# Kernel tuning notes

Measured on AMD Instinct MI355X. Metric: run time of the kernel, lower is better.

The kernel has to match this reference:

```python
import jax, jax.numpy as jnp
import numpy as np

N = 100000  # nodes
E = 1600000  # edges

def gcn_layer(x, W, b, src, tgt, ew):
    # support = x @ W + b ; messages gathered at src, weighted scatter-sum into tgt
    h = x @ W + b                      # [N, F_out]
    msg = h[src] * ew[:, None]         # [E, F_out]
    return jax.ops.segment_sum(msg, tgt, num_segments=N)  # [N, F_out]

def setup_inputs() -> dict:
    key = jax.random.key(0)
    ks = jax.random.split(key, 12)
    nfeat, nhid, nclass = 256, 128, 40
    x = jax.random.normal(ks[0], (N, nfeat), dtype=jnp.float32)
    src = jax.random.randint(ks[1], (E,), 0, N)
    tgt = jax.random.randint(ks[2], (E,), 0, N)
    edge_weight = jax.random.uniform(ks[3], (E,), dtype=jnp.float32)
    def w(k, fi, fo):
        return jax.random.normal(k, (fi, fo), dtype=jnp.float32) / np.sqrt(fi)
    return {
        "x": x, "src": src, "tgt": tgt, "edge_weight": edge_weight,
        "W0": w(ks[4], nfeat, nhid), "b0": jnp.zeros((nhid,), jnp.float32),
        "W1": w(ks[5], nhid, nhid),  "b1": jnp.zeros((nhid,), jnp.float32),
        "W2": w(ks[6], nhid, nhid),  "b2": jnp.zeros((nhid,), jnp.float32),
        "W3": w(ks[7], nhid, nclass),"b3": jnp.zeros((nclass,), jnp.float32),
    }

def reference(x, src, tgt, edge_weight, W0, b0, W1, b1, W2, b2, W3, b3):
    # RESK2 with nlayers=4, eval mode (dropout = identity).
    # x0 = relu(gc0); r = x0; x1 = relu(gc1); x2 = relu(gc2) + r; out = log_softmax(gc3)
    x0 = jax.nn.relu(gcn_layer(x, W0, b0, src, tgt, edge_weight))
    r = x0
    x1 = jax.nn.relu(gcn_layer(x0, W1, b1, src, tgt, edge_weight))
    x2 = jax.nn.relu(gcn_layer(x1, W2, b2, src, tgt, edge_weight)) + r
    logits = gcn_layer(x2, W3, b3, src, tgt, edge_weight)
    return jax.nn.log_softmax(logits, axis=1)
```

## Files before the change

### kernel.cpp

```cpp
#include <hip/hip_runtime.h>
#include <hip/hip_bf16.h>


typedef __attribute__((ext_vector_type(8))) short short8;
typedef __attribute__((ext_vector_type(4))) float float4v;

#define SC_SHIFT 8
#define SC_NODES 256
#define FILL_CAP 12288
#define SRC_MASK 0x1FFFF

static __device__ __forceinline__ float bf2f_lo(unsigned int v) {
    return __uint_as_float(v << 16);
}
static __device__ __forceinline__ float bf2f_hi(unsigned int v) {
    return __uint_as_float(v & 0xffff0000u);
}
static __device__ __forceinline__ unsigned short f2bf(float f) {
    unsigned int u = __float_as_uint(f);
    u = (u + 0x7fffu + ((u >> 16) & 1u)) >> 16;
    return (unsigned short)u;
}
static __device__ __forceinline__ unsigned int packbf(float a, float b) {
    return (unsigned int)f2bf(a) | ((unsigned int)f2bf(b) << 16);
}
static __device__ __forceinline__ float pw_w(unsigned int pe) {
    return __uint_as_float((pe >> 17) << 16);
}

static __device__ __forceinline__ void acc8(float* acc, uint4 v, float wt) {
    acc[0] = fmaf(bf2f_lo(v.x), wt, acc[0]);
    acc[1] = fmaf(bf2f_hi(v.x), wt, acc[1]);
    acc[2] = fmaf(bf2f_lo(v.y), wt, acc[2]);
    acc[3] = fmaf(bf2f_hi(v.y), wt, acc[3]);
    acc[4] = fmaf(bf2f_lo(v.z), wt, acc[4]);
    acc[5] = fmaf(bf2f_hi(v.z), wt, acc[5]);
    acc[6] = fmaf(bf2f_lo(v.w), wt, acc[6]);
    acc[7] = fmaf(bf2f_hi(v.w), wt, acc[7]);
}
static __device__ __forceinline__ void acc4(float* acc, uint2 v, float wt) {
    acc[0] = fmaf(bf2f_lo(v.x), wt, acc[0]);
    acc[1] = fmaf(bf2f_hi(v.x), wt, acc[1]);
    acc[2] = fmaf(bf2f_lo(v.y), wt, acc[2]);
    acc[3] = fmaf(bf2f_hi(v.y), wt, acc[3]);
}

__global__ __launch_bounds__(256) void k_count(const int* __restrict__ tgt,
                                               int* __restrict__ chunkTot,
                                               int E, int NSC) {
    __shared__ int hist[512];
    const int tid = threadIdx.x;
    hist[tid] = 0;
    hist[tid + 256] = 0;
    __syncthreads();
#pragma unroll
    for (int r = 0; r < 4; r++) {
        int e = blockIdx.x * 4096 + r * 1024 + tid * 4;
        if (e + 3 < E) {
            int4 tv = *(const int4*)&tgt[e];
            atomicAdd(&hist[tv.x >> SC_SHIFT], 1);
            atomicAdd(&hist[tv.y >> SC_SHIFT], 1);
            atomicAdd(&hist[tv.z >> SC_SHIFT], 1);
            atomicAdd(&hist[tv.w >> SC_SHIFT], 1);
        } else {
            for (int j = 0; j < 4; j++)
                if (e + j < E) atomicAdd(&hist[tgt[e + j] >> SC_SHIFT], 1);
        }
    }
    __syncthreads();
    for (int i = tid; i < NSC; i += 256) {
        int c = hist[i];
        if (c) atomicAdd(&chunkTot[i], c);
    }
}

__global__ __launch_bounds__(512) void k_scanB(const int* __restrict__ chunkTot,
                                               int* __restrict__ chunkStart,
                                               int* __restrict__ chunkCur,
                                               int E, int NSC) {
    __shared__ int sm[512];
    const int tid = threadIdx.x;
    int v = (tid < NSC) ? chunkTot[tid] : 0;
    sm[tid] = v;
    __syncthreads();
    for (int off = 1; off < 512; off <<= 1) {
        int t = (tid >= off) ? sm[tid - off] : 0;
        __syncthreads();
        sm[tid] += t;
        __syncthreads();
    }
    int excl = sm[tid] - v;
    if (tid < NSC) {
        chunkStart[tid] = excl;
        chunkCur[tid * 32] = excl;
    }
    if (tid == 0) chunkStart[NSC] = E;
}

__global__ __launch_bounds__(512) void k_bucket(const int* __restrict__ src,
                                                const int* __restrict__ tgt,
                                                const float* __restrict__ ew,
                                                int* __restrict__ chunkCur,
                                                unsigned int* __restrict__ st_pw,
                                                unsigned char* __restrict__ st_t8,
                                                int E) {
    __shared__ int cnt[512];
    __shared__ int rk[512];
    __shared__ int bbase[512];
    const int tid = threadIdx.x;
    cnt[tid] = 0;
    rk[tid] = 0;
    __syncthreads();

    int t16[16];
    unsigned int p16[16];
#pragma unroll
    for (int r = 0; r < 4; r++) {
        int e = blockIdx.x * 8192 + r * 2048 + tid * 4;
        if (e + 3 < E) {
            int4 tv = *(const int4*)&tgt[e];
            int4 sv = *(const int4*)&src[e];
            float4 wv = *(const float4*)&ew[e];
            t16[r * 4 + 0] = tv.x; t16[r * 4 + 1] = tv.y;
            t16[r * 4 + 2] = tv.z; t16[r * 4 + 3] = tv.w;
            p16[r * 4 + 0] = ((unsigned int)f2bf(wv.x) << 17) | (unsigned int)sv.x;
            p16[r * 4 + 1] = ((unsigned int)f2bf(wv.y) << 17) | (unsigned int)sv.y;
            p16[r * 4 + 2] = ((unsigned int)f2bf(wv.z) << 17) | (unsigned int)sv.z;
            p16[r * 4 + 3] = ((unsigned int)f2bf(wv.w) << 17) | (unsigned int)sv.w;
        } else {
            for (int j = 0; j < 4; j++) {
                int ee = e + j;
                t16[r * 4 + j] = (ee < E) ? tgt[ee] : -1;
                p16[r * 4 + j] = (ee < E)
                    ? (((unsigned int)f2bf(ew[ee]) << 17) | (unsigned int)src[ee])
                    : 0u;
            }
        }
    }
#pragma unroll
    for (int j = 0; j < 16; j++)
        if (t16[j] >= 0) atomicAdd(&cnt[t16[j] >> SC_SHIFT], 1);
    __syncthreads();
    {
        int c = cnt[tid];
        bbase[tid] = c ? atomicAdd(&chunkCur[tid * 32], c) : 0;
    }
    __syncthreads();
#pragma unroll
    for (int j = 0; j < 16; j++) {
        if (t16[j] >= 0) {
            int c = t16[j] >> SC_SHIFT;
            int pos = bbase[c] + atomicAdd(&rk[c], 1);
            st_pw[pos] = p16[j];
            st_t8[pos] = (unsigned char)(t16[j] & (SC_NODES - 1));
        }
    }
}

__global__ __launch_bounds__(256) void k_fill2(const unsigned int* __restrict__ st_pw,
                                               const unsigned char* __restrict__ st_t8,
                                               const int* __restrict__ chunkStart,
                                               int* __restrict__ rowptr,
                                               unsigned int* __restrict__ perm,
                                               int N, int E, int NSC) {
    __shared__ int lhist[SC_NODES];
    __shared__ int lcur[SC_NODES];
    __shared__ unsigned int ledge[FILL_CAP];
    const int tid = threadIdx.x;
    const int b = blockIdx.x;
    const int n0 = b << SC_SHIFT;
    const int nlocal = min(SC_NODES, N - n0);
    const int sstart = chunkStart[b];
    const int send = chunkStart[b + 1];
    const int cnt = send - sstart;

    lhist[tid] = 0;
    __syncthreads();
    for (int e = sstart + tid; e < send; e += 256)
        atomicAdd(&lhist[st_t8[e]], 1);
    __syncthreads();
    int v = lhist[tid];
    __syncthreads();
    lhist[tid] = v;
    __syncthreads();
    for (int off = 1; off < 256; off <<= 1) {
        int t = (tid >= off) ? lhist[tid - off] : 0;
        __syncthreads();
        lhist[tid] += t;
        __syncthreads();
    }
    int excl = lhist[tid] - v;
    if (tid < nlocal) rowptr[n0 + tid] = sstart + excl;
    if (b == NSC - 1 && tid == 0) rowptr[N] = E;
    lcur[tid] = excl;
    __syncthreads();

    if (cnt <= FILL_CAP) {
        for (int e = sstart + tid; e < send; e += 256) {
            int lt = st_t8[e];
            int pos = atomicAdd(&lcur[lt], 1);
            ledge[pos] = st_pw[e];
        }
        __syncthreads();
        for (int i = tid; i < cnt; i += 256) perm[sstart + i] = ledge[i];
    } else {
        for (int e = sstart + tid; e < send; e += 256) {
            int lt = st_t8[e];
            int pos = atomicAdd(&lcur[lt], 1);
            perm[sstart + pos] = st_pw[e];
        }
    }
}

__global__ __launch_bounds__(256) void k_wtrans_all(
    const float* __restrict__ W0, const float* __restrict__ W1,
    const float* __restrict__ W2, const float* __restrict__ W3,
    unsigned short* __restrict__ Wt0, unsigned short* __restrict__ Wt1,
    unsigned short* __restrict__ Wt2, unsigned short* __restrict__ Wt3,
    int* __restrict__ chunkTot) {
    int idx = blockIdx.x * 256 + threadIdx.x;
    if (idx < 512) chunkTot[idx] = 0;
    if (idx < 32768) {
        int c = idx >> 8, k = idx & 255;
        Wt0[idx] = f2bf(W0[k * 128 + c]);
    } else if (idx < 49152) {
        int i = idx - 32768;
        int c = i >> 7, k = i & 127;
        Wt1[i] = f2bf(W1[k * 128 + c]);
    } else if (idx < 65536) {
        int i = idx - 49152;
        int c = i >> 7, k = i & 127;
        Wt2[i] = f2bf(W2[k * 128 + c]);
    } else if (idx < 71680) {
        int i = idx - 65536;
        int c = i >> 7, k = i & 127;
        Wt3[i] = (c < 40) ? f2bf(W3[k * 40 + c]) : 0;
    }
}

__global__ __launch_bounds__(256) void k_gemm0_mfma(const float* __restrict__ A32,
                                                    const unsigned short* __restrict__ Wt,
                                                    const float* __restrict__ bias,
                                                    unsigned short* __restrict__ C, int N) {
    const int K = 256;
    __shared__ union {
        struct {
            unsigned short As[128 * 40];
            unsigned short Bs[128 * 40];
        } s;
        unsigned short Cs[128 * 136];
    } u;
    __shared__ float bsh[128];
    const int tid = threadIdx.x;
    const int wave = tid >> 6, lane = tid & 63;
    const int quad = lane >> 4, l15 = lane & 15;
    const int rowBase = blockIdx.x * 128;

    if (tid < 128) bsh[tid] = bias[tid];

    const int r0 = tid >> 1, kh = (tid & 1) * 16;
    int rg0 = rowBase + r0;
    rg0 = rg0 < N ? rg0 : N - 1;

    uint4 pa0, pa1, pb0, pb1;
    auto load_step = [&](int k0) {
        const float* ap = &A32[(size_t)rg0 * K + k0 + kh];
        float4 f0 = *(const float4*)&ap[0];
        float4 f1 = *(const float4*)&ap[4];
        float4 f2 = *(const float4*)&ap[8];
        float4 f3 = *(const float4*)&ap[12];
        pa0.x = packbf(f0.x, f0.y); pa0.y = packbf(f0.z, f0.w);
        pa0.z = packbf(f1.x, f1.y); pa0.w = packbf(f1.z, f1.w);
        pa1.x = packbf(f2.x, f2.y); pa1.y = packbf(f2.z, f2.w);
        pa1.z = packbf(f3.x, f3.y); pa1.w = packbf(f3.z, f3.w);
        const unsigned short* bp = &Wt[(size_t)r0 * K + k0 + kh];
        pb0 = *(const uint4*)&bp[0];
        pb1 = *(const uint4*)&bp[8];
    };

    const float4v z = {0.f, 0.f, 0.f, 0.f};
    float4v acc0[8], acc1[8];
#pragma unroll
    for (int j = 0; j < 8; j++) { acc0[j] = z; acc1[j] = z; }

    load_step(0);
    for (int k0 = 0; k0 < K; k0 += 32) {
        *(uint4*)&u.s.As[r0 * 40 + kh] = pa0;
        *(uint4*)&u.s.As[r0 * 40 + kh + 8] = pa1;
        *(uint4*)&u.s.Bs[r0 * 40 + kh] = pb0;
        *(uint4*)&u.s.Bs[r0 * 40 + kh + 8] = pb1;
        __syncthreads();
        if (k0 + 32 < K) load_step(k0 + 32);

        short8 a0 = *(const short8*)&u.s.As[(wave * 32 + l15) * 40 + quad * 8];
        short8 a1 = *(const short8*)&u.s.As[(wave * 32 + 16 + l15) * 40 + quad * 8];
#pragma unroll
        for (int c = 0; c < 8; c++) {
            short8 b = *(const short8*)&u.s.Bs[(c * 16 + l15) * 40 + quad * 8];
            acc0[c] = __builtin_amdgcn_mfma_f32_16x16x32_bf16(b, a0, acc0[c], 0, 0, 0);
            acc1[c] = __builtin_amdgcn_mfma_f32_16x16x32_bf16(b, a1, acc1[c], 0, 0, 0);
        }
        __syncthreads();
    }

#pragma unroll
    for (int c = 0; c < 8; c++) {
        int colBase = c * 16 + quad * 4;
        float4 bv = *(const float4*)&bsh[colBase];
        uint2 o0, o1;
        o0.x = packbf(acc0[c][0] + bv.x, acc0[c][1] + bv.y);
        o0.y = packbf(acc0[c][2] + bv.z, acc0[c][3] + bv.w);
        o1.x = packbf(acc1[c][0] + bv.x, acc1[c][1] + bv.y);
        o1.y = packbf(acc1[c][2] + bv.z, acc1[c][3] + bv.w);
        *(uint2*)&u.Cs[(wave * 32 + l15) * 136 + colBase] = o0;
        *(uint2*)&u.Cs[(wave * 32 + 16 + l15) * 136 + colBase] = o1;
    }
    __syncthreads();
#pragma unroll
    for (int i = 0; i < 8; i++) {
        int flat = i * 256 + tid;
        int row = flat >> 4, q = flat & 15;
        int grow = rowBase + row;
        if (grow < N) {
            uint4 v = *(const uint4*)&u.Cs[row * 136 + q * 8];
            *(uint4*)&C[(size_t)grow * 128 + q * 8] = v;
        }
    }
}

template <int SAVE_RESID>
__global__ __launch_bounds__(512, 4) void k_agg_gemm(
    const unsigned short* __restrict__ h,
    const int* __restrict__ rowptr,
    const unsigned int* __restrict__ perm,
    const unsigned short* __restrict__ Wt,
    const float* __restrict__ bias,
    unsigned short* __restrict__ resid_out,
    unsigned short* __restrict__ C, int N) {
    __shared__ unsigned short As[128 * 136];
    __shared__ unsigned short Bs[128 * 136];
    __shared__ float bsh[128];
    const int tid = threadIdx.x;
    const int wave = tid >> 6, lane = tid & 63;
    const int quad = lane >> 4, l15 = lane & 15;
    const int g = lane >> 4, l = lane & 15;
    const int rowBase = blockIdx.x * 128;

#pragma unroll
    for (int i = 0; i < 4; i++) {
        int flat = i * 512 + tid;
        int row = flat >> 4, kc = flat & 15;
        *(uint4*)&Bs[row * 136 + kc * 8] = *(const uint4*)&Wt[row * 128 + kc * 8];
    }
    if (tid < 128) bsh[tid] = bias[tid];

    const char* hB = (const char*)h;
    const unsigned int loff = (unsigned int)l * 16u;
    for (int nn = 0; nn < 16; nn++) {
        const int nodeRow = wave * 16 + nn;
        int node = rowBase + nodeRow;
        const bool valid = node < N;
        if (!valid) node = N - 1;
        const int beg = rowptr[node], end = rowptr[node + 1];

        float acc[8] = {};
        int base = beg;
        for (; base + 16 <= end; base += 16) {
            unsigned int p0 = perm[base + g];
            unsigned int p1 = perm[base + g + 4];
            unsigned int p2 = perm[base + g + 8];
            unsigned int p3 = perm[base + g + 12];
            uint4 a0 = *(const uint4*)(hB + ((((p0 & SRC_MASK) << 8)) | loff));
            uint4 a1 = *(const uint4*)(hB + ((((p1 & SRC_MASK) << 8)) | loff));
            uint4 a2 = *(const uint4*)(hB + ((((p2 & SRC_MASK) << 8)) | loff));
            uint4 a3 = *(const uint4*)(hB + ((((p3 & SRC_MASK) << 8)) | loff));
            acc8(acc, a0, pw_w(p0));
            acc8(acc, a1, pw_w(p1));
            acc8(acc, a2, pw_w(p2));
            acc8(acc, a3, pw_w(p3));
        }
        const int rem = end - base;
        if (rem > 0) {
            const int last = end - 1;
            auto step = [&](int b4) {
                int e = b4 + g;
                unsigned int p = perm[e <= last ? e : last];
                uint4 a = *(const uint4*)(hB + ((((p & SRC_MASK) << 8)) | loff));
                float w = e <= last ? pw_w(p) : 0.f;
                acc8(acc, a, w);
            };
            step(base);
            if (rem > 4) step(base + 4);
            if (rem > 8) step(base + 8);
            if (rem > 12) step(base + 12);
        }

#pragma unroll
        for (int i = 0; i < 8; i++) {
            acc[i] += __shfl_xor(acc[i], 16);
            acc[i] += __shfl_xor(acc[i], 32);
        }

        if (g == 0) {
#pragma unroll
            for (int i = 0; i < 8; i++) acc[i] = fmaxf(acc[i], 0.f);
            uint4 o;
            o.x = packbf(acc[0], acc[1]);
            o.y = packbf(acc[2], acc[3]);
            o.z = packbf(acc[4], acc[5]);
            o.w = packbf(acc[6], acc[7]);
            *(uint4*)&As[nodeRow * 136 + l * 8] = o;
            if (SAVE_RESID && valid)
                *(uint4*)&resid_out[(size_t)node * 128 + l * 8] = o;
        }
    }
    __syncthreads();

    const float4v z = {0.f, 0.f, 0.f, 0.f};
    float4v acc0[8];
#pragma unroll
    for (int j = 0; j < 8; j++) acc0[j] = z;

#pragma unroll
    for (int k0 = 0; k0 < 128; k0 += 32) {
        short8 a = *(const short8*)&As[(wave * 16 + l15) * 136 + k0 + quad * 8];
#pragma unroll
        for (int c = 0; c < 8; c++) {
            short8 b = *(const short8*)&Bs[(c * 16 + l15) * 136 + k0 + quad * 8];
            acc0[c] = __builtin_amdgcn_mfma_f32_16x16x32_bf16(b, a, acc0[c], 0, 0, 0);
        }
    }
    __syncthreads();

#pragma unroll
    for (int c = 0; c < 8; c++) {
        int colBase = c * 16 + quad * 4;
        float4 bv = *(const float4*)&bsh[colBase];
        uint2 o;
        o.x = packbf(acc0[c][0] + bv.x, acc0[c][1] + bv.y);
        o.y = packbf(acc0[c][2] + bv.z, acc0[c][3] + bv.w);
        *(uint2*)&As[(wave * 16 + l15) * 136 + colBase] = o;
    }
    __syncthreads();
#pragma unroll
    for (int i = 0; i < 4; i++) {
        int flat = i * 512 + tid;
        int row = flat >> 4, q = flat & 15;
        int grow = rowBase + row;
        if (grow < N) {
            uint4 v = *(const uint4*)&As[row * 136 + q * 8];
            *(uint4*)&C[(size_t)grow * 128 + q * 8] = v;
        }
    }
}

__global__ __launch_bounds__(512, 4) void k_agg_gemm40(
    const unsigned short* __restrict__ h,
    const int* __restrict__ rowptr,
    const unsigned int* __restrict__ perm,
    const unsigned short* __restrict__ resid,
    const unsigned short* __restrict__ Wt3,
    const float* __restrict__ bias,
    unsigned short* __restrict__ C, int N) {
    __shared__ unsigned short As[128 * 136];
    __shared__ unsigned short Bs[48 * 136];
    __shared__ float bsh[48];
    const int tid = threadIdx.x;
    const int wave = tid >> 6, lane = tid & 63;
    const int quad = lane >> 4, l15 = lane & 15;
    const int g = lane >> 4, l = lane & 15;
    const int rowBase = blockIdx.x * 128;

    for (int t = tid; t < 48 * 16; t += 512) {
        int row = t >> 4, kc = t & 15;
        *(uint4*)&Bs[row * 136 + kc * 8] = *(const uint4*)&Wt3[row * 128 + kc * 8];
    }
    if (tid < 48) bsh[tid] = (tid < 40) ? bias[tid] : 0.f;

    const char* hB = (const char*)h;
    const unsigned int loff = (unsigned int)l * 16u;
    for (int nn = 0; nn < 16; nn++) {
        const int nodeRow = wave * 16 + nn;
        int node = rowBase + nodeRow;
        const bool valid = node < N;
        if (!valid) node = N - 1;
        const int beg = rowptr[node], end = rowptr[node + 1];

        float acc[8] = {};
        int base = beg;
        for (; base + 16 <= end; base += 16) {
            unsigned int p0 = perm[base + g];
            unsigned int p1 = perm[base + g + 4];
            unsigned int p2 = perm[base + g + 8];
            unsigned int p3 = perm[base + g + 12];
            uint4 a0 = *(const uint4*)(hB + ((((p0 & SRC_MASK) << 8)) | loff));
            uint4 a1 = *(const uint4*)(hB + ((((p1 & SRC_MASK) << 8)) | loff));
            uint4 a2 = *(const uint4*)(hB + ((((p2 & SRC_MASK) << 8)) | loff));
            uint4 a3 = *(const uint4*)(hB + ((((p3 & SRC_MASK) << 8)) | loff));
            acc8(acc, a0, pw_w(p0));
            acc8(acc, a1, pw_w(p1));
            acc8(acc, a2, pw_w(p2));
            acc8(acc, a3, pw_w(p3));
        }
        const int rem = end - base;
        if (rem > 0) {
            const int last = end - 1;
            auto step = [&](int b4) {
                int e = b4 + g;
                unsigned int p = perm[e <= last ? e : last];
                uint4 a = *(const uint4*)(hB + ((((p & SRC_MASK) << 8)) | loff));
                float w = e <= last ? pw_w(p) : 0.f;
                acc8(acc, a, w);
            };
            step(base);
            if (rem > 4) step(base + 4);
            if (rem > 8) step(base + 8);
            if (rem > 12) step(base + 12);
        }

#pragma unroll
        for (int i = 0; i < 8; i++) {
            acc[i] += __shfl_xor(acc[i], 16);
            acc[i] += __shfl_xor(acc[i], 32);
        }

        if (g == 0) {
#pragma unroll
            for (int i = 0; i < 8; i++) acc[i] = fmaxf(acc[i], 0.f);
            uint4 rv = *(const uint4*)&resid[(size_t)node * 128 + l * 8];
            acc[0] += bf2f_lo(rv.x); acc[1] += bf2f_hi(rv.x);
            acc[2] += bf2f_lo(rv.y); acc[3] += bf2f_hi(rv.y);
            acc[4] += bf2f_lo(rv.z); acc[5] += bf2f_hi(rv.z);
            acc[6] += bf2f_lo(rv.w); acc[7] += bf2f_hi(rv.w);
            uint4 o;
            o.x = packbf(acc[0], acc[1]);
            o.y = packbf(acc[2], acc[3]);
            o.z = packbf(acc[4], acc[5]);
            o.w = packbf(acc[6], acc[7]);
            *(uint4*)&As[nodeRow * 136 + l * 8] = o;
        }
    }
    __syncthreads();

    const float4v z = {0.f, 0.f, 0.f, 0.f};
    float4v acc0[3];
#pragma unroll
    for (int j = 0; j < 3; j++) acc0[j] = z;

#pragma unroll
    for (int k0 = 0; k0 < 128; k0 += 32) {
        short8 a = *(const short8*)&As[(wave * 16 + l15) * 136 + k0 + quad * 8];
#pragma unroll
        for (int c = 0; c < 3; c++) {
            short8 b = *(const short8*)&Bs[(c * 16 + l15) * 136 + k0 + quad * 8];
            acc0[c] = __builtin_amdgcn_mfma_f32_16x16x32_bf16(b, a, acc0[c], 0, 0, 0);
        }
    }
    __syncthreads();

    unsigned short* Cs = As;
#pragma unroll
    for (int c = 0; c < 3; c++) {
        int colBase = c * 16 + quad * 4;
        if (c < 2 || quad < 2) {
            float4 bv = *(const float4*)&bsh[colBase];
            uint2 o;
            o.x = packbf(acc0[c][0] + bv.x, acc0[c][1] + bv.y);
            o.y = packbf(acc0[c][2] + bv.z, acc0[c][3] + bv.w);
            *(uint2*)&Cs[(wave * 16 + l15) * 40 + colBase] = o;
        }
    }
    __syncthreads();
#pragma unroll
    for (int i = 0; i < 2; i++) {
        int flat = i * 512 + tid;
        if (flat < 640) {
            int row = flat / 5, q = flat - row * 5;
            int grow = rowBase + row;
            if (grow < N) {
                uint4 v = *(const uint4*)&Cs[row * 40 + q * 8];
                *(uint4*)&C[(size_t)grow * 40 + q * 8] = v;
            }
        }
    }
}

__global__ __launch_bounds__(256) void k_agg40_lsm(const unsigned short* __restrict__ h,
                                                   const int* __restrict__ rowptr,
                                                   const unsigned int* __restrict__ perm,
                                                   float* __restrict__ out, int N) {
    int node = (blockIdx.x * 256 + threadIdx.x) >> 6;
    if (node >= N) return;
    const int lane = threadIdx.x & 63;
    const int g = lane >> 4, l = lane & 15;
    const int beg = rowptr[node], end = rowptr[node + 1];
    const int lc = l < 10 ? l : 0;
    const char* hB = (const char*)h;
    const unsigned int loff = (unsigned int)lc * 8u;

    float acc[4] = {};

    int base = beg;
    for (; base + 16 <= end; base += 16) {
        unsigned int p0 = perm[base + g];
        unsigned int p1 = perm[base + g + 4];
        unsigned int p2 = perm[base + g + 8];
        unsigned int p3 = perm[base + g + 12];
        uint2 a0 = *(const uint2*)(hB + ((p0 & SRC_MASK) * 80u + loff));
        uint2 a1 = *(const uint2*)(hB + ((p1 & SRC_MASK) * 80u + loff));
        uint2 a2 = *(const uint2*)(hB + ((p2 & SRC_MASK) * 80u + loff));
        uint2 a3 = *(const uint2*)(hB + ((p3 & SRC_MASK) * 80u + loff));
        acc4(acc, a0, pw_w(p0));
        acc4(acc, a1, pw_w(p1));
        acc4(acc, a2, pw_w(p2));
        acc4(acc, a3, pw_w(p3));
    }
    const int rem = end - base;
    if (rem > 0) {
        const int last = end - 1;
        auto step = [&](int b4) {
            int e = b4 + g;
            unsigned int p = perm[e <= last ? e : last];
            uint2 a = *(const uint2*)(hB + ((p & SRC_MASK) * 80u + loff));
            float w = e <= last ? pw_w(p) : 0.f;
            acc4(acc, a, w);
        };
        step(base);
        if (rem > 4) step(base + 4);
        if (rem > 8) step(base + 8);
        if (rem > 12) step(base + 12);
    }
#pragma unroll
    for (int i = 0; i < 4; i++) {
        acc[i] += __shfl_xor(acc[i], 16);
        acc[i] += __shfl_xor(acc[i], 32);
    }

    bool vf = l < 10;
    float m = vf ? fmaxf(fmaxf(acc[0], acc[1]), fmaxf(acc[2], acc[3]))
                 : -__builtin_inff();
#pragma unroll
    for (int off = 1; off < 16; off <<= 1) m = fmaxf(m, __shfl_xor(m, off));
    float s = vf ? (expf(acc[0] - m) + expf(acc[1] - m) +
                    expf(acc[2] - m) + expf(acc[3] - m))
                 : 0.f;
#pragma unroll
    for (int off = 1; off < 16; off <<= 1) s += __shfl_xor(s, off);
    float ls = m + logf(s);
    if (g == 0 && vf) {
        float4 o = make_float4(acc[0] - ls, acc[1] - ls, acc[2] - ls, acc[3] - ls);
        *(float4*)&out[(size_t)node * 40 + l * 4] = o;
    }
}

extern "C" void kernel_launch(void* const* d_in, const int* in_sizes, int n_in,
                              void* d_out, int out_size, void* d_ws, size_t ws_size,
                              hipStream_t stream) {
    const float* x  = (const float*)d_in[0];
    const int*   src = (const int*)d_in[1];
    const int*   tgt = (const int*)d_in[2];
    const float* ew  = (const float*)d_in[3];
    const float* W0 = (const float*)d_in[4];
    const float* b0 = (const float*)d_in[5];
    const float* W1 = (const float*)d_in[6];
    const float* b1 = (const float*)d_in[7];
    const float* W2 = (const float*)d_in[8];
    const float* b2 = (const float*)d_in[9];
    const float* W3 = (const float*)d_in[10];
    const float* b3 = (const float*)d_in[11];

    const int N = in_sizes[0] / 256;
    const int E = in_sizes[1];
    const int NSC = (N + SC_NODES - 1) >> SC_SHIFT;

    char* ws = (char*)d_ws;
    size_t off = 0;
    auto alloc = [&](size_t bytes) -> void* {
        void* p = ws + off;
        off = (off + bytes + 255) & ~(size_t)255;
        return p;
    };
    size_t hbytes = (size_t)N * 128 * 2;
    size_t sbytes = (size_t)E * 5 + 256;
    char* hbuf = (char*)alloc(hbytes > sbytes ? hbytes : sbytes);
    unsigned short* Hb = (unsigned short*)hbuf;
    unsigned int* st_pw = (unsigned int*)hbuf;
    unsigned char* st_t8 = (unsigned char*)(hbuf + (size_t)E * 4);
    char* buf1 = (char*)alloc((size_t)N * 128 * 2);
    unsigned short* XAb  = (unsigned short*)buf1;
    char* buf2 = (char*)alloc((size_t)N * 128 * 2);
    unsigned short* XBb  = (unsigned short*)buf2;
    unsigned short* H40b = (unsigned short*)buf2;
    int*   rowptr    = (int*)alloc((size_t)(N + 1) * 4);
    int*   chunkTot  = (int*)alloc(512 * 4);
    int*   chunkStart= (int*)alloc(520 * 4);
    int*   chunkCur  = (int*)alloc(512 * 32 * 4);
    unsigned int* perm = (unsigned int*)alloc((size_t)E * 4);
    unsigned short* Wt0 = (unsigned short*)alloc(256 * 128 * 2);
    unsigned short* Wt1 = (unsigned short*)alloc(128 * 128 * 2);
    unsigned short* Wt2 = (unsigned short*)alloc(128 * 128 * 2);
    unsigned short* Wt3 = (unsigned short*)alloc(48 * 128 * 2);
    (void)ws_size;

    float* logits = (float*)d_out;

    k_wtrans_all<<<(71680 + 255) / 256, 256, 0, stream>>>(W0, W1, W2, W3,
                                                          Wt0, Wt1, Wt2, Wt3,
                                                          chunkTot);
    k_count<<<(E + 4095) / 4096, 256, 0, stream>>>(tgt, chunkTot, E, NSC);
    k_scanB<<<1, 512, 0, stream>>>(chunkTot, chunkStart, chunkCur, E, NSC);
    k_bucket<<<(E + 8191) / 8192, 512, 0, stream>>>(src, tgt, ew, chunkCur,
                                                    st_pw, st_t8, E);
    k_fill2<<<NSC, 256, 0, stream>>>(st_pw, st_t8, chunkStart, rowptr, perm,
                                     N, E, NSC);

    const int gGemm = (N + 127) / 128;
    const int gWave = (N + 3) / 4;

    k_gemm0_mfma<<<gGemm, 256, 0, stream>>>(x, Wt0, b0, Hb, N);
    k_agg_gemm<1><<<gGemm, 512, 0, stream>>>(Hb, rowptr, perm, Wt1, b1, XAb, XBb, N);
    k_agg_gemm<0><<<gGemm, 512, 0, stream>>>(XBb, rowptr, perm, Wt2, b2, nullptr, Hb, N);
    k_agg_gemm40<<<gGemm, 512, 0, stream>>>(Hb, rowptr, perm, XAb, Wt3, b3, H40b, N);
    k_agg40_lsm<<<gWave, 256, 0, stream>>>(H40b, rowptr, perm, logits, N);
}
```

Before: 597.8 us.

## Halve row tiles, drop LDS weight staging, read MFMA weights from global

The fused aggregate+GEMM kernels and the first GEMM now process 64-row tiles with 256-thread blocks instead of 128 rows with 512 threads. The agg kernels no longer copy the weight matrix into shared memory; B fragments are loaded directly from global/L2. Block-wide barriers that only guarded per-wave rows are removed. The aim is less LDS per block, more resident blocks and finer load balance over irregular node degrees. The cost is repeated global weight reads per wave and less weight reuse in the first GEMM.

```diff
diff --git a/kernel.cpp b/kernel.cpp
--- a/kernel.cpp
+++ b/kernel.cpp
@@ -245,60 +245,55 @@
     const int K = 256;
     __shared__ union {
         struct {
-            unsigned short As[128 * 40];
+            unsigned short As[64 * 40];
             unsigned short Bs[128 * 40];
         } s;
-        unsigned short Cs[128 * 136];
+        unsigned short Cs[64 * 136];
     } u;
     __shared__ float bsh[128];
     const int tid = threadIdx.x;
     const int wave = tid >> 6, lane = tid & 63;
     const int quad = lane >> 4, l15 = lane & 15;
-    const int rowBase = blockIdx.x * 128;
+    const int rowBase = blockIdx.x * 64;
 
     if (tid < 128) bsh[tid] = bias[tid];
 
-    const int r0 = tid >> 1, kh = (tid & 1) * 16;
+    const int r0 = tid >> 2, kc0 = tid & 3;
+    const int rB1 = r0, rB2 = r0 + 64;
     int rg0 = rowBase + r0;
     rg0 = rg0 < N ? rg0 : N - 1;
 
-    uint4 pa0, pa1, pb0, pb1;
+    uint4 pa, pb0, pb1;
     auto load_step = [&](int k0) {
-        const float* ap = &A32[(size_t)rg0 * K + k0 + kh];
+        const float* ap = &A32[(size_t)rg0 * K + k0 + kc0 * 8];
         float4 f0 = *(const float4*)&ap[0];
         float4 f1 = *(const float4*)&ap[4];
-        float4 f2 = *(const float4*)&ap[8];
-        float4 f3 = *(const float4*)&ap[12];
-        pa0.x = packbf(f0.x, f0.y); pa0.y = packbf(f0.z, f0.w);
-        pa0.z = packbf(f1.x, f1.y); pa0.w = packbf(f1.z, f1.w);
-        pa1.x = packbf(f2.x, f2.y); pa1.y = packbf(f2.z, f2.w);
-        pa1.z = packbf(f3.x, f3.y); pa1.w = packbf(f3.z, f3.w);
-        const unsigned short* bp = &Wt[(size_t)r0 * K + k0 + kh];
-        pb0 = *(const uint4*)&bp[0];
-        pb1 = *(const uint4*)&bp[8];
+        pa.x = packbf(f0.x, f0.y);
+        pa.y = packbf(f0.z, f0.w);
+        pa.z = packbf(f1.x, f1.y);
+        pa.w = packbf(f1.z, f1.w);
+        pb0 = *(const uint4*)&Wt[(size_t)rB1 * K + k0 + kc0 * 8];
+        pb1 = *(const uint4*)&Wt[(size_t)rB2 * K + k0 + kc0 * 8];
     };
 
     const float4v z = {0.f, 0.f, 0.f, 0.f};
-    float4v acc0[8], acc1[8];
-#pragma unroll
-    for (int j = 0; j < 8; j++) { acc0[j] = z; acc1[j] = z; }
+    float4v acc[8];
+#pragma unroll
+    for (int j = 0; j < 8; j++) acc[j] = z;
 
     load_step(0);
     for (int k0 = 0; k0 < K; k0 += 32) {
-        *(uint4*)&u.s.As[r0 * 40 + kh] = pa0;
-        *(uint4*)&u.s.As[r0 * 40 + kh + 8] = pa1;
-        *(uint4*)&u.s.Bs[r0 * 40 + kh] = pb0;
-        *(uint4*)&u.s.Bs[r0 * 40 + kh + 8] = pb1;
+        *(uint4*)&u.s.As[r0 * 40 + kc0 * 8] = pa;
+        *(uint4*)&u.s.Bs[rB1 * 40 + kc0 * 8] = pb0;
+        *(uint4*)&u.s.Bs[rB2 * 40 + kc0 * 8] = pb1;
         __syncthreads();
         if (k0 + 32 < K) load_step(k0 + 32);
 
-        short8 a0 = *(const short8*)&u.s.As[(wave * 32 + l15) * 40 + quad * 8];
-        short8 a1 = *(const short8*)&u.s.As[(wave * 32 + 16 + l15) * 40 + quad * 8];
+        short8 a = *(const short8*)&u.s.As[(wave * 16 + l15) * 40 + quad * 8];
 #pragma unroll
         for (int c = 0; c < 8; c++) {
             short8 b = *(const short8*)&u.s.Bs[(c * 16 + l15) * 40 + quad * 8];
-            acc0[c] = __builtin_amdgcn_mfma_f32_16x16x32_bf16(b, a0, acc0[c], 0, 0, 0);
-            acc1[c] = __builtin_amdgcn_mfma_f32_16x16x32_bf16(b, a1, acc1[c], 0, 0, 0);
+            acc[c] = __builtin_amdgcn_mfma_f32_16x16x32_bf16(b, a, acc[c], 0, 0, 0);
         }
         __syncthreads();
     }
@@ -307,17 +302,14 @@
     for (int c = 0; c < 8; c++) {
         int colBase = c * 16 + quad * 4;
         float4 bv = *(const float4*)&bsh[colBase];
-        uint2 o0, o1;
-        o0.x = packbf(acc0[c][0] + bv.x, acc0[c][1] + bv.y);
-        o0.y = packbf(acc0[c][2] + bv.z, acc0[c][3] + bv.w);
-        o1.x = packbf(acc1[c][0] + bv.x, acc1[c][1] + bv.y);
-        o1.y = packbf(acc1[c][2] + bv.z, acc1[c][3] + bv.w);
-        *(uint2*)&u.Cs[(wave * 32 + l15) * 136 + colBase] = o0;
-        *(uint2*)&u.Cs[(wave * 32 + 16 + l15) * 136 + colBase] = o1;
-    }
-    __syncthreads();
-#pragma unroll
-    for (int i = 0; i < 8; i++) {
+        uint2 o;
+        o.x = packbf(acc[c][0] + bv.x, acc[c][1] + bv.y);
+        o.y = packbf(acc[c][2] + bv.z, acc[c][3] + bv.w);
+        *(uint2*)&u.Cs[(wave * 16 + l15) * 136 + colBase] = o;
+    }
+    __syncthreads();
+#pragma unroll
+    for (int i = 0; i < 4; i++) {
         int flat = i * 256 + tid;
         int row = flat >> 4, q = flat & 15;
         int grow = rowBase + row;
@@ -329,7 +321,7 @@
 }
 
 template <int SAVE_RESID>
-__global__ __launch_bounds__(512, 4) void k_agg_gemm(
+__global__ __launch_bounds__(256) void k_agg_gemm(
     const unsigned short* __restrict__ h,
     const int* __restrict__ rowptr,
     const unsigned int* __restrict__ perm,
@@ -337,21 +329,14 @@
     const float* __restrict__ bias,
     unsigned short* __restrict__ resid_out,
     unsigned short* __restrict__ C, int N) {
-    __shared__ unsigned short As[128 * 136];
-    __shared__ unsigned short Bs[128 * 136];
+    __shared__ unsigned short As[64 * 136];
     __shared__ float bsh[128];
     const int tid = threadIdx.x;
     const int wave = tid >> 6, lane = tid & 63;
     const int quad = lane >> 4, l15 = lane & 15;
     const int g = lane >> 4, l = lane & 15;
-    const int rowBase = blockIdx.x * 128;
-
-#pragma unroll
-    for (int i = 0; i < 4; i++) {
-        int flat = i * 512 + tid;
-        int row = flat >> 4, kc = flat & 15;
-        *(uint4*)&Bs[row * 136 + kc * 8] = *(const uint4*)&Wt[row * 128 + kc * 8];
-    }
+    const int rowBase = blockIdx.x * 64;
+
     if (tid < 128) bsh[tid] = bias[tid];
 
     const char* hB = (const char*)h;
@@ -414,7 +399,6 @@
                 *(uint4*)&resid_out[(size_t)node * 128 + l * 8] = o;
         }
     }
-    __syncthreads();
 
     const float4v z = {0.f, 0.f, 0.f, 0.f};
     float4v acc0[8];
@@ -426,11 +410,10 @@
         short8 a = *(const short8*)&As[(wave * 16 + l15) * 136 + k0 + quad * 8];
 #pragma unroll
         for (int c = 0; c < 8; c++) {
-            short8 b = *(const short8*)&Bs[(c * 16 + l15) * 136 + k0 + quad * 8];
+            short8 b = *(const short8*)&Wt[(c * 16 + l15) * 128 + k0 + quad * 8];
             acc0[c] = __builtin_amdgcn_mfma_f32_16x16x32_bf16(b, a, acc0[c], 0, 0, 0);
         }
     }
-    __syncthreads();
 
 #pragma unroll
     for (int c = 0; c < 8; c++) {
@@ -444,7 +427,7 @@
     __syncthreads();
 #pragma unroll
     for (int i = 0; i < 4; i++) {
-        int flat = i * 512 + tid;
+        int flat = i * 256 + tid;
         int row = flat >> 4, q = flat & 15;
         int grow = rowBase + row;
         if (grow < N) {
@@ -454,7 +437,7 @@
     }
 }
 
-__global__ __launch_bounds__(512, 4) void k_agg_gemm40(
+__global__ __launch_bounds__(256) void k_agg_gemm40(
     const unsigned short* __restrict__ h,
     const int* __restrict__ rowptr,
     const unsigned int* __restrict__ perm,
@@ -462,19 +445,14 @@
     const unsigned short* __restrict__ Wt3,
     const float* __restrict__ bias,
     unsigned short* __restrict__ C, int N) {
-    __shared__ unsigned short As[128 * 136];
-    __shared__ unsigned short Bs[48 * 136];
+    __shared__ unsigned short As[64 * 136];
     __shared__ float bsh[48];
     const int tid = threadIdx.x;
     const int wave = tid >> 6, lane = tid & 63;
     const int quad = lane >> 4, l15 = lane & 15;
     const int g = lane >> 4, l = lane & 15;
-    const int rowBase = blockIdx.x * 128;
-
-    for (int t = tid; t < 48 * 16; t += 512) {
-        int row = t >> 4, kc = t & 15;
-        *(uint4*)&Bs[row * 136 + kc * 8] = *(const uint4*)&Wt3[row * 128 + kc * 8];
-    }
+    const int rowBase = blockIdx.x * 64;
+
     if (tid < 48) bsh[tid] = (tid < 40) ? bias[tid] : 0.f;
 
     const char* hB = (const char*)h;
@@ -540,7 +518,6 @@
             *(uint4*)&As[nodeRow * 136 + l * 8] = o;
         }
     }
-    __syncthreads();
 
     const float4v z = {0.f, 0.f, 0.f, 0.f};
     float4v acc0[3];
@@ -552,7 +529,7 @@
         short8 a = *(const short8*)&As[(wave * 16 + l15) * 136 + k0 + quad * 8];
 #pragma unroll
         for (int c = 0; c < 3; c++) {
-            short8 b = *(const short8*)&Bs[(c * 16 + l15) * 136 + k0 + quad * 8];
+            short8 b = *(const short8*)&Wt3[(c * 16 + l15) * 128 + k0 + quad * 8];
             acc0[c] = __builtin_amdgcn_mfma_f32_16x16x32_bf16(b, a, acc0[c], 0, 0, 0);
         }
     }
@@ -573,8 +550,8 @@
     __syncthreads();
 #pragma unroll
     for (int i = 0; i < 2; i++) {
-        int flat = i * 512 + tid;
-        if (flat < 640) {
+        int flat = i * 256 + tid;
+        if (flat < 320) {
             int row = flat / 5, q = flat - row * 5;
             int grow = rowBase + row;
             if (grow < N) {
@@ -714,12 +691,12 @@
     k_fill2<<<NSC, 256, 0, stream>>>(st_pw, st_t8, chunkStart, rowptr, perm,
                                      N, E, NSC);
 
-    const int gGemm = (N + 127) / 128;
+    const int gTile = (N + 63) / 64;
     const int gWave = (N + 3) / 4;
 
-    k_gemm0_mfma<<<gGemm, 256, 0, stream>>>(x, Wt0, b0, Hb, N);
-    k_agg_gemm<1><<<gGemm, 512, 0, stream>>>(Hb, rowptr, perm, Wt1, b1, XAb, XBb, N);
-    k_agg_gemm<0><<<gGemm, 512, 0, stream>>>(XBb, rowptr, perm, Wt2, b2, nullptr, Hb, N);
-    k_agg_gemm40<<<gGemm, 512, 0, stream>>>(Hb, rowptr, perm, XAb, Wt3, b3, H40b, N);
+    k_gemm0_mfma<<<gTile, 256, 0, stream>>>(x, Wt0, b0, Hb, N);
+    k_agg_gemm<1><<<gTile, 256, 0, stream>>>(Hb, rowptr, perm, Wt1, b1, XAb, XBb, N);
+    k_agg_gemm<0><<<gTile, 256, 0, stream>>>(XBb, rowptr, perm, Wt2, b2, nullptr, Hb, N);
+    k_agg_gemm40<<<gTile, 256, 0, stream>>>(Hb, rowptr, perm, XAb, Wt3, b3, H40b, N);
     k_agg40_lsm<<<gWave, 256, 0, stream>>>(H40b, rowptr, perm, logits, N);
 }
```

Result: slower. 610.0 us (+2.1%).
